# Performance work log

Measured on AMD Instinct MI355X. Metric: run time of the kernel, lower is better.

## Reference

```python
import math
import jax, jax.numpy as jnp
import numpy as np

# dims (from init_kwargs / forward signature)
B, N, K = 8, 1024, 8            # batch, nodes, num_neighbors
NC, TED, TEC = 64, 128, 64      # num_channels, time_embedding_dim, time_embedding_channels
C = NC + TEC                    # model dim = 128
H, Dh = 8, 16                   # heads, dim_head
HD = H * Dh
L = 4                           # num_layers
RH = 32                         # radial-net hidden width
NPATH = 10                      # radial scalars: k00,k10,k01,k11a,k11b,v00,v10,v01,v11a,v11b


def _g(k, shape, fan_in):
    return jax.random.normal(k, shape, dtype=jnp.float32) / np.sqrt(float(fan_in))


def setup_inputs() -> dict:
    key = jax.random.key(0)
    ks = jax.random.split(key, 16)
    return dict(
        x=jax.random.normal(ks[0], (B, N, 3), dtype=jnp.float32),
        y=jax.random.normal(ks[1], (B, N, 3), dtype=jnp.float32),
        t=jax.random.uniform(ks[2], (B,), dtype=jnp.float32) * 1000.0,
        Wt1=_g(ks[3], (TED, TED), TED), bt1=jnp.zeros((TED,), jnp.float32),
        Wt2=_g(ks[4], (TED, TEC), TED), bt2=jnp.zeros((TEC,), jnp.float32),
        Win0=_g(ks[5], (TEC + 3, C), TEC + 3), bin0=jnp.zeros((C,), jnp.float32),
        Win1=_g(ks[6], (1, C), 1),
        Wqkv=_g(ks[7], (L, 12, C, HD), C),           # q0,q1,k00,k10,k01,k11a,k11b,v00,v10,v01,v11a,v11b
        Wr1=_g(ks[8], (L, 1, RH), 1), br1=jnp.zeros((L, RH), jnp.float32),
        Wr2=_g(ks[9], (L, RH, H * NPATH), RH), br2=jnp.zeros((L, H * NPATH), jnp.float32),
        Wo=_g(ks[10], (L, 2, HD, C), HD), bo=jnp.zeros((L, 2, C), jnp.float32),
        Wout=_g(ks[11], (3, C), C), bout=jnp.zeros((3,), jnp.float32),
    )


def _forward(x, y, t, Wt1, bt1, Wt2, bt2, Win0, bin0, Win1, Wqkv,
             Wr1, br1, Wr2, br2, Wo, bo, Wout, bout):
    b, n = x.shape[0], x.shape[1]
    # sinusoidal time embedding + time MLP
    half = TED // 2
    freqs = jnp.exp(-math.log(10000.0) * jnp.arange(half, dtype=x.dtype) / half)
    emb = t[:, None] * freqs
    temb = jnp.concatenate([jnp.sin(emb), jnp.cos(emb)], axis=-1)          # [B,TED]
    temb = jax.nn.silu(temb @ Wt1 + bt1) @ Wt2 + bt2                        # [B,TEC]

    # degree-0 input = [time_embed | coords], degree-1 input = coords (1 channel)
    deg0 = jnp.concatenate([jnp.broadcast_to(temb[:, None, :], (b, n, TEC)), x], axis=-1)
    f0 = deg0 @ Win0 + bin0                                                 # [B,N,C]
    f1 = jnp.einsum('bnv,c->bncv', x, Win1[0])                              # [B,N,C,3]

    # k-nearest-neighbor graph on coordinates (shared across layers)
    d2 = jnp.sum((x[:, :, None, :] - x[:, None, :, :]) ** 2, axis=-1)       # [B,N,N]
    d2 = d2 + jnp.eye(n, dtype=x.dtype) * 1e9                               # exclude self
    _, idx = jax.lax.top_k(-d2, K)                                          # [B,N,K]
    gather = lambda f: jax.vmap(lambda a, i: a[i])(f, idx)                  # [B,N,...] -> [B,N,K,...]
    rel = gather(x) - x[:, :, None, :]                                      # [B,N,K,3]
    r = jnp.sqrt(jnp.sum(rel ** 2, axis=-1, keepdims=True) + 1e-8)          # [B,N,K,1]
    rhat = rel / r

    inv_scale = 1.0 / float(np.sqrt(2 * Dh))
    for l in range(L):
        Wl = Wqkv[l].reshape(12, C, H, Dh)
        q0 = jnp.einsum('bnc,chd->bnhd', f0, Wl[0])
        q1 = jnp.einsum('bncv,chd->bnhdv', f1, Wl[1])
        f0j, f1j = gather(f0), gather(f1)                                   # [B,N,K,C], [B,N,K,C,3]
        # radial network -> per-head, per-path scalars
        Rn = (jax.nn.silu(r @ Wr1[l] + br1[l]) @ Wr2[l] + br2[l]).reshape(b, n, K, H, NPATH)
        # equivariant tensor-product paths (degrees 0/1, spherical harmonics Y0,Y1,Y2)
        dot1 = jnp.einsum('bnkcv,bnkv->bnkc', f1j, rhat)                    # 1->0 path
        sym = 3.0 * dot1[..., None] * rhat[:, :, :, None, :] - f1j          # Y2 (traceless sym) 1->1 path
        p0 = lambda f, w: jnp.einsum('bnkc,chd->bnkhd', f, w)
        p1 = lambda f, w: jnp.einsum('bnkcv,chd->bnkhdv', f, w)
        rh = rhat[:, :, :, None, None, :]
        k0 = p0(f0j, Wl[2]) * Rn[..., 0:1] + p0(dot1, Wl[3]) * Rn[..., 1:2]
        k1 = (p0(f0j, Wl[4])[..., None] * rh * Rn[..., 2][..., None, None]
              + p1(f1j, Wl[5]) * Rn[..., 3][..., None, None]
              + p1(sym, Wl[6]) * Rn[..., 4][..., None, None])
        v0 = p0(f0j, Wl[7]) * Rn[..., 5:6] + p0(dot1, Wl[8]) * Rn[..., 6:7]
        v1 = (p0(f0j, Wl[9])[..., None] * rh * Rn[..., 7][..., None, None]
              + p1(f1j, Wl[10]) * Rn[..., 8][..., None, None]
              + p1(sym, Wl[11]) * Rn[..., 9][..., None, None])
        logits = (jnp.einsum('bnhd,bnkhd->bnhk', q0, k0)
                  + jnp.einsum('bnhdv,bnkhdv->bnhk', q1, k1)) * inv_scale
        attn = jax.nn.softmax(logits, axis=-1)
        o0 = jnp.einsum('bnhk,bnkhd->bnhd', attn, v0).reshape(b, n, HD)
        o1 = jnp.einsum('bnhk,bnkhdv->bnhdv', attn, v1).reshape(b, n, HD, 3)
        f0 = f0 + o0 @ Wo[l, 0] + bo[l, 0]
        f1 = f1 + jnp.einsum('bnev,ec->bncv', o1, Wo[l, 1]) + bo[l, 1][None, None, :, None]

    # output layer Linear(dim, 3) applied as per-component channel mixing on the type-1 output
    return jnp.einsum('bncv,vc->bnv', f1, Wout) + bout                      # [B,N,3]


def reference(x, y, t, Wt1, bt1, Wt2, bt2, Win0, bin0, Win1, Wqkv,
              Wr1, br1, Wr2, br2, Wo, bo, Wout, bout):
    return _forward(x, y, t, Wt1, bt1, Wt2, bt2, Win0, bin0, Win1, Wqkv,
                    Wr1, br1, Wr2, br2, Wo, bo, Wout, bout)
```

## Files before the change

kernel.cpp:

```cpp
#include <hip/hip_runtime.h>
#include <math.h>

#define NBATCH 8
#define NPTS   1024
#define KNN    8
#define CC     128
#define HD_    128
#define TED_   128
#define TEC_   64
#define RH     32
#define NL     4

typedef _Float16 half8 __attribute__((ext_vector_type(8)));
typedef _Float16 h4v  __attribute__((ext_vector_type(4)));
typedef float f32x4 __attribute__((ext_vector_type(4)));

__global__ __launch_bounds__(128) void k_temb(
    const float* __restrict__ t, const float* __restrict__ Wt1,
    const float* __restrict__ bt1, const float* __restrict__ Wt2,
    const float* __restrict__ bt2, const float* __restrict__ Win0,
    const float* __restrict__ bin0, float* __restrict__ pre0)
{
  int b = blockIdx.x;
  int tid = threadIdx.x;
  __shared__ float e128[TED_];
  __shared__ float h1[TED_];
  __shared__ float te[TEC_];
  float tv = t[b];
  if (tid < 64) {
    float fr = expf((-9.210340371976184f * (float)tid) * 0.015625f);
    float em = tv * fr;
    e128[tid]      = sinf(em);
    e128[tid + 64] = cosf(em);
  }
  __syncthreads();
  {
    float acc = bt1[tid];
    for (int i = 0; i < TED_; ++i) acc += e128[i] * Wt1[i * TED_ + tid];
    h1[tid] = acc / (1.0f + expf(-acc));
  }
  __syncthreads();
  if (tid < TEC_) {
    float acc = bt2[tid];
    for (int j = 0; j < TED_; ++j) acc += h1[j] * Wt2[j * TEC_ + tid];
    te[tid] = acc;
  }
  __syncthreads();
  {
    float acc = bin0[tid];
    for (int i = 0; i < TEC_; ++i) acc += te[i] * Win0[i * CC + tid];
    pre0[b * CC + tid] = acc;
  }
}

__global__ __launch_bounds__(256) void k_init(
    const float* __restrict__ x, const float* __restrict__ Win0,
    const float* __restrict__ Win1, const float* __restrict__ pre0,
    float* __restrict__ f0, float* __restrict__ f1,
    _Float16* __restrict__ f0h, _Float16* __restrict__ f1h)
{
  int node = blockIdx.x * 2 + (threadIdx.x >> 7);
  int c = threadIdx.x & 127;
  int b = node >> 10;
  float x0 = x[node * 3 + 0], x1 = x[node * 3 + 1], x2 = x[node * 3 + 2];
  float acc = pre0[b * CC + c]
            + x0 * Win0[(TEC_ + 0) * CC + c]
            + x1 * Win0[(TEC_ + 1) * CC + c]
            + x2 * Win0[(TEC_ + 2) * CC + c];
  f0[(size_t)node * CC + c] = acc;
  f0h[(size_t)node * CC + c] = (_Float16)acc;
  float w1 = Win1[c];
  float v0 = x0 * w1, v1 = x1 * w1, v2 = x2 * w1;
  f1[((size_t)node * 3 + 0) * CC + c] = v0;
  f1[((size_t)node * 3 + 1) * CC + c] = v1;
  f1[((size_t)node * 3 + 2) * CC + c] = v2;
  f1h[((size_t)node * 3 + 0) * CC + c] = (_Float16)v0;
  f1h[((size_t)node * 3 + 1) * CC + c] = (_Float16)v1;
  f1h[((size_t)node * 3 + 2) * CC + c] = (_Float16)v2;
}

__global__ __launch_bounds__(256) void k_knn(
    const float* __restrict__ x, int* __restrict__ idx,
    float* __restrict__ rhat, float* __restrict__ rl)
{
  const int b    = blockIdx.x >> 8;
  const int tile = blockIdx.x & 255;
  const int tid  = threadIdx.x;
  const int qg   = tid >> 6;
  const int sub  = tid & 63;

  __shared__ float xsx[NPTS], xsy[NPTS], xsz[NPTS];

  for (int i = tid; i < NPTS; i += 256) {
    const float* xp = x + ((size_t)b * NPTS + i) * 3;
    xsx[i] = xp[0]; xsy[i] = xp[1]; xsz[i] = xp[2];
  }
  __syncthreads();

  const int n = tile * 4 + qg;
  const float qx = xsx[n], qy = xsy[n], qz = xsz[n];

  unsigned long long bd[KNN];
  #pragma unroll
  for (int k = 0; k < KNN; ++k) bd[k] = ~0ull;

  const int j0 = sub * 16;
  #pragma unroll
  for (int it = 0; it < 16; ++it) {
    int j = j0 + ((it + sub) & 15);
    float dx = qx - xsx[j];
    float dy = qy - xsy[j];
    float dz = qz - xsz[j];
    float s = __fadd_rn(__fadd_rn(__fmul_rn(dx, dx), __fmul_rn(dy, dy)),
                        __fmul_rn(dz, dz));
    if (j == n) s = 1.0e9f;
    unsigned long long key =
        ((unsigned long long)__float_as_uint(s) << 32) | (unsigned int)j;
    if (key < bd[KNN - 1]) {
      bd[KNN - 1] = key;
      #pragma unroll
      for (int q = KNN - 1; q > 0; --q) {
        if (bd[q] < bd[q - 1]) {
          unsigned long long tmp = bd[q]; bd[q] = bd[q - 1]; bd[q - 1] = tmp;
        }
      }
    }
  }

  unsigned long long res[KNN];
  #pragma unroll
  for (int r = 0; r < KNN; ++r) {
    unsigned long long m = bd[0];
    #pragma unroll
    for (int mk = 1; mk < 64; mk <<= 1) {
      unsigned long long o = (unsigned long long)__shfl_xor((long long)m, mk, 64);
      m = (o < m) ? o : m;
    }
    if (bd[0] == m) {
      #pragma unroll
      for (int q = 0; q < KNN - 1; ++q) bd[q] = bd[q + 1];
      bd[KNN - 1] = ~0ull;
    }
    res[r] = m;
  }

  if (sub < KNN) {
    unsigned long long key = res[0];
    #pragma unroll
    for (int r = 1; r < KNN; ++r) if (sub == r) key = res[r];
    int j = (int)(key & 0xffffffffu);
    size_t base = ((size_t)b * NPTS + n) * KNN + sub;
    idx[base] = j;
    float rx = xsx[j] - qx;
    float ry = xsy[j] - qy;
    float rz = xsz[j] - qz;
    float rr2 = rx * rx + ry * ry + rz * rz + 1e-8f;
    float r = sqrtf(rr2);
    rl[base] = r;
    rhat[base * 3 + 0] = rx / r;
    rhat[base * 3 + 1] = ry / r;
    rhat[base * 3 + 2] = rz / r;
  }
}

__global__ __launch_bounds__(256) void k_rn(
    const float* __restrict__ rl, const float* __restrict__ Wr1,
    const float* __restrict__ br1, const float* __restrict__ Wr2,
    const float* __restrict__ br2, _Float16* __restrict__ Rn)
{
  const int l = blockIdx.y;
  const int e0 = blockIdx.x * 64;
  const int t = threadIdx.x;
  __shared__ _Float16 hid[64][48];
  __shared__ _Float16 wt[80][48];
  __shared__ _Float16 rn_lds[64][128];

  {
    uint4 zz = {0, 0, 0, 0};
    #pragma unroll
    for (int u = 0; u < 4; ++u)
      *(uint4*)((char*)rn_lds + (u * 256 + t) * 16) = zz;
  }
  {
    const float* wr2 = Wr2 + l * RH * 80;
    for (int i = t; i < 2560; i += 256) {
      int n = i >> 5, k = i & 31;
      wt[n][k] = (_Float16)wr2[k * 80 + n];
    }
  }
  {
    const float* wr1 = Wr1 + l * RH;
    const float* wb1 = br1 + l * RH;
    int e = t >> 2, i0 = (t & 3) * 8;
    float rv = rl[e0 + e];
    #pragma unroll
    for (int q = 0; q < 8; ++q) {
      int i = i0 + q;
      float zv = rv * wr1[i] + wb1[i];
      hid[e][i] = (_Float16)(zv / (1.0f + expf(-zv)));
    }
  }
  __syncthreads();

  {
    const int lane = t & 63;
    const int w = t >> 6;
    const int r15 = lane & 15;
    const int g = lane >> 4;
    half8 af = *(const half8*)&hid[w * 16 + r15][g * 8];
    const float* wb2 = br2 + l * 80;
    #pragma unroll
    for (int nt = 0; nt < 5; ++nt) {
      half8 bf = *(const half8*)&wt[nt * 16 + r15][g * 8];
      f32x4 acc = {};
      acc = __builtin_amdgcn_mfma_f32_16x16x32_f16(af, bf, acc, 0, 0, 0);
      int col = nt * 16 + r15;
      int hh = col / 10, j = col - hh * 10;
      float bv = wb2[col];
      #pragma unroll
      for (int i = 0; i < 4; ++i) {
        int e = w * 16 + g * 4 + i;
        rn_lds[e][hh * 16 + j] = (_Float16)(acc[i] + bv);
      }
    }
  }
  __syncthreads();
  _Float16* dst = Rn + ((size_t)l * 65536 + e0) * 128;
  #pragma unroll
  for (int u = 0; u < 4; ++u) {
    int i = u * 256 + t;
    *(uint4*)(dst + i * 8) = *(const uint4*)((const char*)rn_lds + i * 16);
  }
}

__global__ __launch_bounds__(256) void k_wconv(
    const float* __restrict__ Wqkv, const float* __restrict__ Wo,
    _Float16* __restrict__ Whq, _Float16* __restrict__ Who)
{
  __shared__ _Float16 T[128][136];
  int m = blockIdx.x;
  const float* src; _Float16* dst;
  if (m < 48) { src = Wqkv + (size_t)m * 16384; dst = Whq + (size_t)m * 16384; }
  else { src = Wo + (size_t)(m - 48) * 16384; dst = Who + (size_t)(m - 48) * 16384; }
  int tid = threadIdx.x;
  for (int i = tid; i < 16384; i += 256) {
    int k = i >> 7, n = i & 127;
    T[n][k] = (_Float16)src[i];
  }
  __syncthreads();
  for (int i = tid; i < 16384; i += 256) {
    int n = i >> 7, k = i & 127;
    dst[i] = T[n][k];
  }
}

#define MFMA_BODY(A_, ROWBASE_, WT_)                                          \
  const int tid  = threadIdx.x;                                               \
  const int lane = tid & 63;                                                  \
  const int w    = tid >> 6;                                                  \
  const int r15  = lane & 15;                                                 \
  const int g    = lane >> 4;                                                 \
  half8 bf[2][4];                                                             \
  _Pragma("unroll")                                                           \
  for (int ntl = 0; ntl < 2; ++ntl) {                                         \
    int n = (w * 2 + ntl) * 16 + r15;                                         \
    const _Float16* wp = (WT_) + (size_t)n * 128 + g * 8;                     \
    _Pragma("unroll")                                                         \
    for (int ks = 0; ks < 4; ++ks)                                            \
      bf[ntl][ks] = *(const half8*)(wp + ks * 32);                            \
  }                                                                           \
  {                                                                           \
    int r = tid >> 1;                                                         \
    const _Float16* src = (A_) + (size_t)((ROWBASE_) + r) * 128;              \
    int c0 = (tid & 1) * 8;                                                   \
    _Pragma("unroll")                                                         \
    for (int q = 0; q < 8; ++q) {                                             \
      int c = c0 + q;                                                         \
      *(uint4*)&As[r][c * 8] = *(const uint4*)(src + c * 8);                  \
    }                                                                         \
  }                                                                           \
  __syncthreads();                                                            \
  f32x4 acc[8][2] = {};                                                       \
  _Pragma("unroll")                                                           \
  for (int ks = 0; ks < 4; ++ks) {                                            \
    half8 a[8];                                                               \
    _Pragma("unroll")                                                         \
    for (int mt = 0; mt < 8; ++mt)                                            \
      a[mt] = *(const half8*)&As[mt * 16 + r15][ks * 32 + g * 8];             \
    _Pragma("unroll")                                                         \
    for (int mt = 0; mt < 8; ++mt) {                                          \
      acc[mt][0] = __builtin_amdgcn_mfma_f32_16x16x32_f16(bf[0][ks], a[mt], acc[mt][0], 0, 0, 0); \
      acc[mt][1] = __builtin_amdgcn_mfma_f32_16x16x32_f16(bf[1][ks], a[mt], acc[mt][1], 0, 0, 0); \
    }                                                                         \
  }

__global__ __launch_bounds__(256) void k_proj_mfma(
    const _Float16* __restrict__ f0h, const _Float16* __restrict__ f1h,
    const _Float16* __restrict__ Wh, _Float16* __restrict__ P0,
    _Float16* __restrict__ P1, int nb0)
{
  __shared__ _Float16 As[128][136];
  int z = blockIdx.x;
  const _Float16* A; const _Float16* Wt; _Float16* P; int ldP, colBase, rowBase;
  if (z < nb0 * 5) {
    const int map0[5] = {0, 2, 4, 7, 9};
    int m = z / nb0, rb = z - m * nb0;
    A = f0h; rowBase = rb * 128;
    Wt = Wh + (size_t)map0[m] * 16384;
    P = P0; ldP = 640; colBase = m * 128;
  } else {
    z -= nb0 * 5;
    int nb1 = nb0 * 3;
    const int map1[7] = {1, 3, 5, 6, 8, 10, 11};
    int m = z / nb1, rb = z - m * nb1;
    A = f1h; rowBase = rb * 128;
    Wt = Wh + (size_t)map1[m] * 16384;
    P = P1; ldP = 896; colBase = m * 128;
  }
  MFMA_BODY(A, rowBase, Wt)
  #pragma unroll
  for (int mt = 0; mt < 8; ++mt) {
    int row = rowBase + mt * 16 + r15;
    #pragma unroll
    for (int ntl = 0; ntl < 2; ++ntl) {
      int col = colBase + (w * 2 + ntl) * 16 + g * 4;
      h4v o;
      #pragma unroll
      for (int i = 0; i < 4; ++i) o[i] = (_Float16)acc[mt][ntl][i];
      *(h4v*)(P + (size_t)row * ldP + col) = o;
    }
  }
}

__global__ __launch_bounds__(256) void k_wo_mfma(
    const _Float16* __restrict__ o0h, const _Float16* __restrict__ o1h,
    const _Float16* __restrict__ Who_l, const float* __restrict__ bo_l,
    float* __restrict__ f0, float* __restrict__ f1,
    _Float16* __restrict__ f0h, _Float16* __restrict__ f1h, int nb0)
{
  __shared__ _Float16 As[128][136];
  int z = blockIdx.x;
  const _Float16* A; const _Float16* Wt; const float* bias;
  float* F; _Float16* FH; int rowBase;
  if (z < nb0) {
    A = o0h; Wt = Who_l; bias = bo_l; F = f0; FH = f0h; rowBase = z * 128;
  } else {
    z -= nb0;
    A = o1h; Wt = Who_l + 16384; bias = bo_l + CC; F = f1; FH = f1h; rowBase = z * 128;
  }
  MFMA_BODY(A, rowBase, Wt)
  #pragma unroll
  for (int mt = 0; mt < 8; ++mt) {
    int row = rowBase + mt * 16 + r15;
    #pragma unroll
    for (int ntl = 0; ntl < 2; ++ntl) {
      int col = (w * 2 + ntl) * 16 + g * 4;
      float4 bv = *(const float4*)&bias[col];
      float* fp = F + (size_t)row * 128 + col;
      _Float16* fhp = FH + (size_t)row * 128 + col;
      float4 fv = *(float4*)fp;
      fv.x += acc[mt][ntl][0] + bv.x;
      fv.y += acc[mt][ntl][1] + bv.y;
      fv.z += acc[mt][ntl][2] + bv.z;
      fv.w += acc[mt][ntl][3] + bv.w;
      *(float4*)fp = fv;
      h4v hh;
      hh[0] = (_Float16)fv.x; hh[1] = (_Float16)fv.y;
      hh[2] = (_Float16)fv.z; hh[3] = (_Float16)fv.w;
      *(h4v*)fhp = hh;
    }
  }
}

__global__ __launch_bounds__(256) void k_attn(
    const _Float16* __restrict__ P0, const _Float16* __restrict__ P1,
    const int* __restrict__ idx, const float* __restrict__ rhat,
    const _Float16* __restrict__ RnL,
    _Float16* __restrict__ o0h, _Float16* __restrict__ o1h,
    int nodeBase, int nbg)
{
  const int t = threadIdx.x;
  const int wv = t >> 6;
  const int lane = t & 63;
  const int cl = lane & 31;
  const int nh = lane >> 5;
  const int z = blockIdx.x;
  const int bb = z % nbg;
  const int qbase = (z / nbg) * 4;
  const int nodeLocal = bb * NPTS + qbase + wv;
  const int node = nodeBase + nodeLocal;
  const int batchRow = bb * NPTS;

  __shared__ float rh_s[4][KNN][3];
  if (t < 96) {
    int nd = t / 24, e = t % 24;
    rh_s[nd][e / 3][e % 3] =
        rhat[((size_t)(nodeBase + bb * NPTS + qbase + nd)) * KNN * 3 + e];
  }
  __syncthreads();

  const int c0 = cl * 4;
  const int h = cl >> 2;
  const _Float16* p0n = P0 + (size_t)nodeLocal * 640 + c0;
  const _Float16* p1n = P1 + (size_t)nodeLocal * 2688 + c0;
  h4v q0v  = *(const h4v*)(p0n);
  h4v q1xv = *(const h4v*)(p1n);
  h4v q1yv = *(const h4v*)(p1n + 896);
  h4v q1zv = *(const h4v*)(p1n + 1792);

  const float inv_scale = 0.17677669529663687f;
  const int* idxp = idx + (size_t)node * KNN + nh * 4;
  int jls[4];
  #pragma unroll
  for (int k = 0; k < 4; ++k) jls[k] = batchRow + idxp[k];
  const _Float16* rnp = RnL + ((size_t)node * KNN + nh * 4) * 128 + h * 16;

  float m = -3.0e38f, ssum = 0.0f;
  float a0[4] = {}, ax[4] = {}, ay[4] = {}, az[4] = {};

  for (int k = 0; k < 4; ++k) {
    int kk = nh * 4 + k;
    int jl = jls[k];
    const _Float16* g0 = P0 + (size_t)jl * 640 + c0;
    const _Float16* g1 = P1 + (size_t)jl * 2688 + c0;
    float rx = rh_s[wv][kk][0], ry = rh_s[wv][kk][1], rz = rh_s[wv][kk][2];

    half8 rv = *(const half8*)(rnp + (size_t)k * 128);
    h4v rv2 = *(const h4v*)(rnp + (size_t)k * 128 + 8);
    float r0 = (float)rv[0], r1 = (float)rv[1], r2 = (float)rv[2], r3 = (float)rv[3];
    float r4 = (float)rv[4], r5 = (float)rv[5], r6 = (float)rv[6], r7 = (float)rv[7];
    float r8 = (float)rv2[0], r9 = (float)rv2[1];

    float pl = 0.0f;
    {
      h4v G02 = *(const h4v*)(g0 + 128), G04 = *(const h4v*)(g0 + 256);
      h4v G13x = *(const h4v*)(g1 + 128),  G13y = *(const h4v*)(g1 + 896 + 128),  G13z = *(const h4v*)(g1 + 1792 + 128);
      h4v G15x = *(const h4v*)(g1 + 256),  G15y = *(const h4v*)(g1 + 896 + 256),  G15z = *(const h4v*)(g1 + 1792 + 256);
      h4v G16x = *(const h4v*)(g1 + 384),  G16y = *(const h4v*)(g1 + 896 + 384),  G16z = *(const h4v*)(g1 + 1792 + 384);
      #pragma unroll
      for (int ci = 0; ci < 4; ++ci) {
        float g02 = (float)G02[ci], g04 = (float)G04[ci];
        float g13x = (float)G13x[ci], g13y = (float)G13y[ci], g13z = (float)G13z[ci];
        float g15x = (float)G15x[ci], g15y = (float)G15y[ci], g15z = (float)G15z[ci];
        float g16x = (float)G16x[ci], g16y = (float)G16y[ci], g16z = (float)G16z[ci];
        float DP3 = g13x * rx + g13y * ry + g13z * rz;
        float DP6 = g16x * rx + g16y * ry + g16z * rz;
        float k0  = g02 * r0 + DP3 * r1;
        float k1x = g04 * rx * r2 + g15x * r3 + (3.0f * rx * DP6 - g16x) * r4;
        float k1y = g04 * ry * r2 + g15y * r3 + (3.0f * ry * DP6 - g16y) * r4;
        float k1z = g04 * rz * r2 + g15z * r3 + (3.0f * rz * DP6 - g16z) * r4;
        pl += (float)q0v[ci] * k0 + (float)q1xv[ci] * k1x
            + (float)q1yv[ci] * k1y + (float)q1zv[ci] * k1z;
      }
    }
    pl += __shfl_xor(pl, 1, 4);
    pl += __shfl_xor(pl, 2, 4);
    pl *= inv_scale;

    float mnew = fmaxf(m, pl);
    float scale = expf(m - mnew);
    float wgt = expf(pl - mnew);
    ssum = ssum * scale + wgt;
    m = mnew;

    {
      h4v G07 = *(const h4v*)(g0 + 384), G09 = *(const h4v*)(g0 + 512);
      h4v G18x = *(const h4v*)(g1 + 512),  G18y = *(const h4v*)(g1 + 896 + 512),  G18z = *(const h4v*)(g1 + 1792 + 512);
      h4v G1Ax = *(const h4v*)(g1 + 640),  G1Ay = *(const h4v*)(g1 + 896 + 640),  G1Az = *(const h4v*)(g1 + 1792 + 640);
      h4v G1Bx = *(const h4v*)(g1 + 768),  G1By = *(const h4v*)(g1 + 896 + 768),  G1Bz = *(const h4v*)(g1 + 1792 + 768);
      #pragma unroll
      for (int ci = 0; ci < 4; ++ci) {
        float g07 = (float)G07[ci], g09 = (float)G09[ci];
        float g18x = (float)G18x[ci], g18y = (float)G18y[ci], g18z = (float)G18z[ci];
        float g1ax = (float)G1Ax[ci], g1ay = (float)G1Ay[ci], g1az = (float)G1Az[ci];
        float g1bx = (float)G1Bx[ci], g1by = (float)G1By[ci], g1bz = (float)G1Bz[ci];
        float DP8 = g18x * rx + g18y * ry + g18z * rz;
        float DPB = g1bx * rx + g1by * ry + g1bz * rz;
        float v0  = g07 * r5 + DP8 * r6;
        float v1x = g09 * rx * r7 + g1ax * r8 + (3.0f * rx * DPB - g1bx) * r9;
        float v1y = g09 * ry * r7 + g1ay * r8 + (3.0f * ry * DPB - g1by) * r9;
        float v1z = g09 * rz * r7 + g1az * r8 + (3.0f * rz * DPB - g1bz) * r9;
        a0[ci] = a0[ci] * scale + wgt * v0;
        ax[ci] = ax[ci] * scale + wgt * v1x;
        ay[ci] = ay[ci] * scale + wgt * v1y;
        az[ci] = az[ci] * scale + wgt * v1z;
      }
    }
  }

  {
    float mo = __shfl_xor(m, 32, 64);
    float so = __shfl_xor(ssum, 32, 64);
    float mn = fmaxf(m, mo);
    float s_self = expf(m - mn);
    float s_oth  = expf(mo - mn);
    ssum = ssum * s_self + so * s_oth;
    #pragma unroll
    for (int ci = 0; ci < 4; ++ci) {
      float o0 = __shfl_xor(a0[ci], 32, 64);
      float ox = __shfl_xor(ax[ci], 32, 64);
      float oy = __shfl_xor(ay[ci], 32, 64);
      float oz = __shfl_xor(az[ci], 32, 64);
      a0[ci] = a0[ci] * s_self + o0 * s_oth;
      ax[ci] = ax[ci] * s_self + ox * s_oth;
      ay[ci] = ay[ci] * s_self + oy * s_oth;
      az[ci] = az[ci] * s_self + oz * s_oth;
    }
  }

  if (nh == 0) {
    float invs = 1.0f / ssum;
    h4v o;
    #pragma unroll
    for (int ci = 0; ci < 4; ++ci) o[ci] = (_Float16)(a0[ci] * invs);
    *(h4v*)(o0h + (size_t)nodeLocal * 128 + c0) = o;
    #pragma unroll
    for (int ci = 0; ci < 4; ++ci) o[ci] = (_Float16)(ax[ci] * invs);
    *(h4v*)(o1h + ((size_t)nodeLocal * 3 + 0) * 128 + c0) = o;
    #pragma unroll
    for (int ci = 0; ci < 4; ++ci) o[ci] = (_Float16)(ay[ci] * invs);
    *(h4v*)(o1h + ((size_t)nodeLocal * 3 + 1) * 128 + c0) = o;
    #pragma unroll
    for (int ci = 0; ci < 4; ++ci) o[ci] = (_Float16)(az[ci] * invs);
    *(h4v*)(o1h + ((size_t)nodeLocal * 3 + 2) * 128 + c0) = o;
  }
}

__global__ __launch_bounds__(256) void k_out(
    const float* __restrict__ f1, const float* __restrict__ Wout,
    const float* __restrict__ bout, float* __restrict__ out)
{
  int i = blockIdx.x * 256 + threadIdx.x;
  int v = i % 3;
  const float* row = f1 + (size_t)i * CC;
  const float* w = Wout + v * CC;
  float acc = 0.0f;
  #pragma unroll
  for (int c = 0; c < CC; c += 4) {
    float4 fv = *(const float4*)&row[c];
    float4 wv = *(const float4*)&w[c];
    acc += fv.x * wv.x + fv.y * wv.y + fv.z * wv.z + fv.w * wv.w;
  }
  out[i] = acc + bout[v];
}

extern "C" void kernel_launch(void* const* d_in, const int* in_sizes, int n_in,
                              void* d_out, int out_size, void* d_ws, size_t ws_size,
                              hipStream_t stream) {
  const float* x    = (const float*)d_in[0];
  const float* t    = (const float*)d_in[2];
  const float* Wt1  = (const float*)d_in[3];
  const float* bt1  = (const float*)d_in[4];
  const float* Wt2  = (const float*)d_in[5];
  const float* bt2  = (const float*)d_in[6];
  const float* Win0 = (const float*)d_in[7];
  const float* bin0 = (const float*)d_in[8];
  const float* Win1 = (const float*)d_in[9];
  const float* Wqkv = (const float*)d_in[10];
  const float* Wr1  = (const float*)d_in[11];
  const float* br1  = (const float*)d_in[12];
  const float* Wr2  = (const float*)d_in[13];
  const float* br2  = (const float*)d_in[14];
  const float* Wo   = (const float*)d_in[15];
  const float* bo   = (const float*)d_in[16];
  const float* Wout = (const float*)d_in[17];
  const float* bout = (const float*)d_in[18];
  float* out = (float*)d_out;

  char* wsb = (char*)d_ws;
  size_t off = 0;
  auto alloc = [&](size_t bytes) -> void* {
    void* p = wsb + off;
    off = (off + bytes + 255) & ~(size_t)255;
    return p;
  };
  const int totalNodes = NBATCH * NPTS;
  float* pre0 = (float*)alloc((size_t)NBATCH * CC * 4);
  float* f0   = (float*)alloc((size_t)totalNodes * CC * 4);
  float* f1   = (float*)alloc((size_t)totalNodes * 3 * CC * 4);
  _Float16* f0h = (_Float16*)alloc((size_t)totalNodes * CC * 2);
  _Float16* f1h = (_Float16*)alloc((size_t)totalNodes * 3 * CC * 2);
  _Float16* Whq = (_Float16*)alloc((size_t)NL * 12 * CC * HD_ * 2);
  _Float16* Who = (_Float16*)alloc((size_t)NL * 2 * CC * HD_ * 2);
  int*   idx  = (int*)alloc((size_t)totalNodes * KNN * 4);
  float* rhat = (float*)alloc((size_t)totalNodes * KNN * 3 * 4);
  float* rl   = (float*)alloc((size_t)totalNodes * KNN * 4);
  _Float16* Rn = (_Float16*)alloc((size_t)NL * totalNodes * KNN * 128 * 2);
  size_t fixedBytes = off;
  size_t perBatch = (size_t)NPTS * ((640 + 2688) * 2 + (128 + 384) * 2);
  int nbg = 8;
  while (nbg > 1 && fixedBytes + (size_t)nbg * perBatch + 8192 > ws_size) nbg >>= 1;
  _Float16* P0  = (_Float16*)alloc((size_t)nbg * NPTS * 640 * 2);
  _Float16* P1  = (_Float16*)alloc((size_t)nbg * NPTS * 2688 * 2);
  _Float16* o0h = (_Float16*)alloc((size_t)nbg * NPTS * 128 * 2);
  _Float16* o1h = (_Float16*)alloc((size_t)nbg * NPTS * 384 * 2);

  k_temb<<<NBATCH, 128, 0, stream>>>(t, Wt1, bt1, Wt2, bt2, Win0, bin0, pre0);
  k_init<<<totalNodes / 2, 256, 0, stream>>>(x, Win0, Win1, pre0, f0, f1, f0h, f1h);
  k_knn<<<NBATCH * 256, 256, 0, stream>>>(x, idx, rhat, rl);
  k_wconv<<<56, 256, 0, stream>>>(Wqkv, Wo, Whq, Who);
  k_rn<<<dim3(totalNodes * KNN / 64, NL), 256, 0, stream>>>(rl, Wr1, br1, Wr2, br2, Rn);

  for (int g = 0; g < NBATCH / nbg; ++g) {
    int nodeBase = g * nbg * NPTS;
    int nodes = nbg * NPTS;
    int nb0 = nodes / 128;
    for (int l = 0; l < NL; ++l) {
      k_proj_mfma<<<nb0 * 26, 256, 0, stream>>>(
          f0h + (size_t)nodeBase * CC, f1h + (size_t)nodeBase * 3 * CC,
          Whq + (size_t)l * 12 * CC * HD_, P0, P1, nb0);
      k_attn<<<nodes / 4, 256, 0, stream>>>(
          P0, P1, idx, rhat, Rn + (size_t)l * totalNodes * KNN * 128,
          o0h, o1h, nodeBase, nbg);
      k_wo_mfma<<<nb0 * 4, 256, 0, stream>>>(
          o0h, o1h, Who + (size_t)l * 2 * CC * HD_, bo + (size_t)(l * 2) * CC,
          f0 + (size_t)nodeBase * CC, f1 + (size_t)nodeBase * 3 * CC,
          f0h + (size_t)nodeBase * CC, f1h + (size_t)nodeBase * 3 * CC, nb0);
    }
  }
  k_out<<<(totalNodes * 3) / 256, 256, 0, stream>>>(f1, Wout, bout, out);
}
```

Measured before the change: 377.8 us.

## Split attention into logit/softmax and value-aggregation kernels

Splits the fused online-softmax attention kernel in two. The first kernel computes logits and normalized softmax weights into a small float buffer. The second kernel gathers values and accumulates them with those precomputed weights. The k-loops are fully unrolled, so more gathered loads can be in flight and the serial online-softmax rescaling goes away. In exchange it adds a kernel launch per layer, a round trip of the weight buffer through memory, and a second read of the index and rhat data.

```diff
diff --git a/kernel.cpp b/kernel.cpp
--- a/kernel.cpp
+++ b/kernel.cpp
@@ -372,11 +372,10 @@
   }
 }
 
-__global__ __launch_bounds__(256) void k_attn(
+__global__ __launch_bounds__(256) void k_attnA(
     const _Float16* __restrict__ P0, const _Float16* __restrict__ P1,
     const int* __restrict__ idx, const float* __restrict__ rhat,
-    const _Float16* __restrict__ RnL,
-    _Float16* __restrict__ o0h, _Float16* __restrict__ o1h,
+    const _Float16* __restrict__ RnL, float* __restrict__ Wgt,
     int nodeBase, int nbg)
 {
   const int t = threadIdx.x;
@@ -415,9 +414,8 @@
   for (int k = 0; k < 4; ++k) jls[k] = batchRow + idxp[k];
   const _Float16* rnp = RnL + ((size_t)node * KNN + nh * 4) * 128 + h * 16;
 
-  float m = -3.0e38f, ssum = 0.0f;
-  float a0[4] = {}, ax[4] = {}, ay[4] = {}, az[4] = {};
-
+  float pls[4];
+  #pragma unroll
   for (int k = 0; k < 4; ++k) {
     int kk = nh * 4 + k;
     int jl = jls[k];
@@ -426,102 +424,151 @@
     float rx = rh_s[wv][kk][0], ry = rh_s[wv][kk][1], rz = rh_s[wv][kk][2];
 
     half8 rv = *(const half8*)(rnp + (size_t)k * 128);
-    h4v rv2 = *(const h4v*)(rnp + (size_t)k * 128 + 8);
-    float r0 = (float)rv[0], r1 = (float)rv[1], r2 = (float)rv[2], r3 = (float)rv[3];
-    float r4 = (float)rv[4], r5 = (float)rv[5], r6 = (float)rv[6], r7 = (float)rv[7];
-    float r8 = (float)rv2[0], r9 = (float)rv2[1];
+    float r0 = (float)rv[0], r1 = (float)rv[1], r2 = (float)rv[2];
+    float r3 = (float)rv[3], r4 = (float)rv[4];
+
+    h4v G02 = *(const h4v*)(g0 + 128), G04 = *(const h4v*)(g0 + 256);
+    h4v G13x = *(const h4v*)(g1 + 128),  G13y = *(const h4v*)(g1 + 1024),  G13z = *(const h4v*)(g1 + 1920);
+    h4v G15x = *(const h4v*)(g1 + 256),  G15y = *(const h4v*)(g1 + 1152),  G15z = *(const h4v*)(g1 + 2048);
+    h4v G16x = *(const h4v*)(g1 + 384),  G16y = *(const h4v*)(g1 + 1280),  G16z = *(const h4v*)(g1 + 2176);
 
     float pl = 0.0f;
-    {
-      h4v G02 = *(const h4v*)(g0 + 128), G04 = *(const h4v*)(g0 + 256);
-      h4v G13x = *(const h4v*)(g1 + 128),  G13y = *(const h4v*)(g1 + 896 + 128),  G13z = *(const h4v*)(g1 + 1792 + 128);
-      h4v G15x = *(const h4v*)(g1 + 256),  G15y = *(const h4v*)(g1 + 896 + 256),  G15z = *(const h4v*)(g1 + 1792 + 256);
-      h4v G16x = *(const h4v*)(g1 + 384),  G16y = *(const h4v*)(g1 + 896 + 384),  G16z = *(const h4v*)(g1 + 1792 + 384);
-      #pragma unroll
-      for (int ci = 0; ci < 4; ++ci) {
-        float g02 = (float)G02[ci], g04 = (float)G04[ci];
-        float g13x = (float)G13x[ci], g13y = (float)G13y[ci], g13z = (float)G13z[ci];
-        float g15x = (float)G15x[ci], g15y = (float)G15y[ci], g15z = (float)G15z[ci];
-        float g16x = (float)G16x[ci], g16y = (float)G16y[ci], g16z = (float)G16z[ci];
-        float DP3 = g13x * rx + g13y * ry + g13z * rz;
-        float DP6 = g16x * rx + g16y * ry + g16z * rz;
-        float k0  = g02 * r0 + DP3 * r1;
-        float k1x = g04 * rx * r2 + g15x * r3 + (3.0f * rx * DP6 - g16x) * r4;
-        float k1y = g04 * ry * r2 + g15y * r3 + (3.0f * ry * DP6 - g16y) * r4;
-        float k1z = g04 * rz * r2 + g15z * r3 + (3.0f * rz * DP6 - g16z) * r4;
-        pl += (float)q0v[ci] * k0 + (float)q1xv[ci] * k1x
-            + (float)q1yv[ci] * k1y + (float)q1zv[ci] * k1z;
-      }
+    #pragma unroll
+    for (int ci = 0; ci < 4; ++ci) {
+      float g02 = (float)G02[ci], g04 = (float)G04[ci];
+      float g13x = (float)G13x[ci], g13y = (float)G13y[ci], g13z = (float)G13z[ci];
+      float g15x = (float)G15x[ci], g15y = (float)G15y[ci], g15z = (float)G15z[ci];
+      float g16x = (float)G16x[ci], g16y = (float)G16y[ci], g16z = (float)G16z[ci];
+      float DP3 = g13x * rx + g13y * ry + g13z * rz;
+      float DP6 = g16x * rx + g16y * ry + g16z * rz;
+      float k0  = g02 * r0 + DP3 * r1;
+      float k1x = g04 * rx * r2 + g15x * r3 + (3.0f * rx * DP6 - g16x) * r4;
+      float k1y = g04 * ry * r2 + g15y * r3 + (3.0f * ry * DP6 - g16y) * r4;
+      float k1z = g04 * rz * r2 + g15z * r3 + (3.0f * rz * DP6 - g16z) * r4;
+      pl += (float)q0v[ci] * k0 + (float)q1xv[ci] * k1x
+          + (float)q1yv[ci] * k1y + (float)q1zv[ci] * k1z;
     }
     pl += __shfl_xor(pl, 1, 4);
     pl += __shfl_xor(pl, 2, 4);
-    pl *= inv_scale;
-
-    float mnew = fmaxf(m, pl);
-    float scale = expf(m - mnew);
-    float wgt = expf(pl - mnew);
-    ssum = ssum * scale + wgt;
-    m = mnew;
-
-    {
-      h4v G07 = *(const h4v*)(g0 + 384), G09 = *(const h4v*)(g0 + 512);
-      h4v G18x = *(const h4v*)(g1 + 512),  G18y = *(const h4v*)(g1 + 896 + 512),  G18z = *(const h4v*)(g1 + 1792 + 512);
-      h4v G1Ax = *(const h4v*)(g1 + 640),  G1Ay = *(const h4v*)(g1 + 896 + 640),  G1Az = *(const h4v*)(g1 + 1792 + 640);
-      h4v G1Bx = *(const h4v*)(g1 + 768),  G1By = *(const h4v*)(g1 + 896 + 768),  G1Bz = *(const h4v*)(g1 + 1792 + 768);
-      #pragma unroll
-      for (int ci = 0; ci < 4; ++ci) {
-        float g07 = (float)G07[ci], g09 = (float)G09[ci];
-        float g18x = (float)G18x[ci], g18y = (float)G18y[ci], g18z = (float)G18z[ci];
-        float g1ax = (float)G1Ax[ci], g1ay = (float)G1Ay[ci], g1az = (float)G1Az[ci];
-        float g1bx = (float)G1Bx[ci], g1by = (float)G1By[ci], g1bz = (float)G1Bz[ci];
-        float DP8 = g18x * rx + g18y * ry + g18z * rz;
-        float DPB = g1bx * rx + g1by * ry + g1bz * rz;
-        float v0  = g07 * r5 + DP8 * r6;
-        float v1x = g09 * rx * r7 + g1ax * r8 + (3.0f * rx * DPB - g1bx) * r9;
-        float v1y = g09 * ry * r7 + g1ay * r8 + (3.0f * ry * DPB - g1by) * r9;
-        float v1z = g09 * rz * r7 + g1az * r8 + (3.0f * rz * DPB - g1bz) * r9;
-        a0[ci] = a0[ci] * scale + wgt * v0;
-        ax[ci] = ax[ci] * scale + wgt * v1x;
-        ay[ci] = ay[ci] * scale + wgt * v1y;
-        az[ci] = az[ci] * scale + wgt * v1z;
-      }
-    }
-  }
-
-  {
-    float mo = __shfl_xor(m, 32, 64);
-    float so = __shfl_xor(ssum, 32, 64);
-    float mn = fmaxf(m, mo);
-    float s_self = expf(m - mn);
-    float s_oth  = expf(mo - mn);
-    ssum = ssum * s_self + so * s_oth;
+    pls[k] = pl * inv_scale;
+  }
+
+  float mh = fmaxf(fmaxf(pls[0], pls[1]), fmaxf(pls[2], pls[3]));
+  float w0 = expf(pls[0] - mh), w1 = expf(pls[1] - mh);
+  float w2 = expf(pls[2] - mh), w3 = expf(pls[3] - mh);
+  float sh = w0 + w1 + w2 + w3;
+
+  float mo = __shfl_xor(mh, 32, 64);
+  float so = __shfl_xor(sh, 32, 64);
+  float mt_ = fmaxf(mh, mo);
+  float st = sh * expf(mh - mt_) + so * expf(mo - mt_);
+  float factor = expf(mh - mt_) / st;
+
+  if ((cl & 3) == 0) {
+    float4 wq;
+    wq.x = w0 * factor; wq.y = w1 * factor;
+    wq.z = w2 * factor; wq.w = w3 * factor;
+    *(float4*)(Wgt + (size_t)nodeLocal * 64 + h * 8 + nh * 4) = wq;
+  }
+}
+
+__global__ __launch_bounds__(256) void k_attnB(
+    const _Float16* __restrict__ P0, const _Float16* __restrict__ P1,
+    const int* __restrict__ idx, const float* __restrict__ rhat,
+    const _Float16* __restrict__ RnL, const float* __restrict__ Wgt,
+    _Float16* __restrict__ o0h, _Float16* __restrict__ o1h,
+    int nodeBase, int nbg)
+{
+  const int t = threadIdx.x;
+  const int wv = t >> 6;
+  const int lane = t & 63;
+  const int cl = lane & 31;
+  const int nh = lane >> 5;
+  const int z = blockIdx.x;
+  const int bb = z % nbg;
+  const int qbase = (z / nbg) * 4;
+  const int nodeLocal = bb * NPTS + qbase + wv;
+  const int node = nodeBase + nodeLocal;
+  const int batchRow = bb * NPTS;
+
+  __shared__ float rh_s[4][KNN][3];
+  if (t < 96) {
+    int nd = t / 24, e = t % 24;
+    rh_s[nd][e / 3][e % 3] =
+        rhat[((size_t)(nodeBase + bb * NPTS + qbase + nd)) * KNN * 3 + e];
+  }
+  __syncthreads();
+
+  const int c0 = cl * 4;
+  const int h = cl >> 2;
+  const int* idxp = idx + (size_t)node * KNN + nh * 4;
+  int jls[4];
+  #pragma unroll
+  for (int k = 0; k < 4; ++k) jls[k] = batchRow + idxp[k];
+  const _Float16* rnp = RnL + ((size_t)node * KNN + nh * 4) * 128 + h * 16;
+  float4 wq = *(const float4*)(Wgt + (size_t)nodeLocal * 64 + h * 8 + nh * 4);
+
+  float a0[4] = {}, ax[4] = {}, ay[4] = {}, az[4] = {};
+
+  #pragma unroll
+  for (int k = 0; k < 4; ++k) {
+    int kk = nh * 4 + k;
+    int jl = jls[k];
+    const _Float16* g0 = P0 + (size_t)jl * 640 + c0;
+    const _Float16* g1 = P1 + (size_t)jl * 2688 + c0;
+    float rx = rh_s[wv][kk][0], ry = rh_s[wv][kk][1], rz = rh_s[wv][kk][2];
+
+    half8 rv = *(const half8*)(rnp + (size_t)k * 128);
+    h4v rv2 = *(const h4v*)(rnp + (size_t)k * 128 + 8);
+    float r5 = (float)rv[5], r6 = (float)rv[6], r7 = (float)rv[7];
+    float r8 = (float)rv2[0], r9 = (float)rv2[1];
+    float wk = (k == 0) ? wq.x : (k == 1) ? wq.y : (k == 2) ? wq.z : wq.w;
+
+    h4v G07 = *(const h4v*)(g0 + 384), G09 = *(const h4v*)(g0 + 512);
+    h4v G18x = *(const h4v*)(g1 + 512),  G18y = *(const h4v*)(g1 + 1408),  G18z = *(const h4v*)(g1 + 2304);
+    h4v G1Ax = *(const h4v*)(g1 + 640),  G1Ay = *(const h4v*)(g1 + 1536),  G1Az = *(const h4v*)(g1 + 2432);
+    h4v G1Bx = *(const h4v*)(g1 + 768),  G1By = *(const h4v*)(g1 + 1664),  G1Bz = *(const h4v*)(g1 + 2560);
+
     #pragma unroll
     for (int ci = 0; ci < 4; ++ci) {
-      float o0 = __shfl_xor(a0[ci], 32, 64);
-      float ox = __shfl_xor(ax[ci], 32, 64);
-      float oy = __shfl_xor(ay[ci], 32, 64);
-      float oz = __shfl_xor(az[ci], 32, 64);
-      a0[ci] = a0[ci] * s_self + o0 * s_oth;
-      ax[ci] = ax[ci] * s_self + ox * s_oth;
-      ay[ci] = ay[ci] * s_self + oy * s_oth;
-      az[ci] = az[ci] * s_self + oz * s_oth;
-    }
+      float g07 = (float)G07[ci], g09 = (float)G09[ci];
+      float g18x = (float)G18x[ci], g18y = (float)G18y[ci], g18z = (float)G18z[ci];
+      float g1ax = (float)G1Ax[ci], g1ay = (float)G1Ay[ci], g1az = (float)G1Az[ci];
+      float g1bx = (float)G1Bx[ci], g1by = (float)G1By[ci], g1bz = (float)G1Bz[ci];
+      float DP8 = g18x * rx + g18y * ry + g18z * rz;
+      float DPB = g1bx * rx + g1by * ry + g1bz * rz;
+      float v0  = g07 * r5 + DP8 * r6;
+      float v1x = g09 * rx * r7 + g1ax * r8 + (3.0f * rx * DPB - g1bx) * r9;
+      float v1y = g09 * ry * r7 + g1ay * r8 + (3.0f * ry * DPB - g1by) * r9;
+      float v1z = g09 * rz * r7 + g1az * r8 + (3.0f * rz * DPB - g1bz) * r9;
+      a0[ci] += wk * v0;
+      ax[ci] += wk * v1x;
+      ay[ci] += wk * v1y;
+      az[ci] += wk * v1z;
+    }
+  }
+
+  #pragma unroll
+  for (int ci = 0; ci < 4; ++ci) {
+    a0[ci] += __shfl_xor(a0[ci], 32, 64);
+    ax[ci] += __shfl_xor(ax[ci], 32, 64);
+    ay[ci] += __shfl_xor(ay[ci], 32, 64);
+    az[ci] += __shfl_xor(az[ci], 32, 64);
   }
 
   if (nh == 0) {
-    float invs = 1.0f / ssum;
     h4v o;
     #pragma unroll
-    for (int ci = 0; ci < 4; ++ci) o[ci] = (_Float16)(a0[ci] * invs);
+    for (int ci = 0; ci < 4; ++ci) o[ci] = (_Float16)a0[ci];
     *(h4v*)(o0h + (size_t)nodeLocal * 128 + c0) = o;
     #pragma unroll
-    for (int ci = 0; ci < 4; ++ci) o[ci] = (_Float16)(ax[ci] * invs);
+    for (int ci = 0; ci < 4; ++ci) o[ci] = (_Float16)ax[ci];
     *(h4v*)(o1h + ((size_t)nodeLocal * 3 + 0) * 128 + c0) = o;
     #pragma unroll
-    for (int ci = 0; ci < 4; ++ci) o[ci] = (_Float16)(ay[ci] * invs);
+    for (int ci = 0; ci < 4; ++ci) o[ci] = (_Float16)ay[ci];
     *(h4v*)(o1h + ((size_t)nodeLocal * 3 + 1) * 128 + c0) = o;
     #pragma unroll
-    for (int ci = 0; ci < 4; ++ci) o[ci] = (_Float16)(az[ci] * invs);
+    for (int ci = 0; ci < 4; ++ci) o[ci] = (_Float16)az[ci];
     *(h4v*)(o1h + ((size_t)nodeLocal * 3 + 2) * 128 + c0) = o;
   }
 }
@@ -587,13 +634,14 @@
   float* rl   = (float*)alloc((size_t)totalNodes * KNN * 4);
   _Float16* Rn = (_Float16*)alloc((size_t)NL * totalNodes * KNN * 128 * 2);
   size_t fixedBytes = off;
-  size_t perBatch = (size_t)NPTS * ((640 + 2688) * 2 + (128 + 384) * 2);
+  size_t perBatch = (size_t)NPTS * ((640 + 2688) * 2 + (128 + 384) * 2 + 64 * 4);
   int nbg = 8;
   while (nbg > 1 && fixedBytes + (size_t)nbg * perBatch + 8192 > ws_size) nbg >>= 1;
   _Float16* P0  = (_Float16*)alloc((size_t)nbg * NPTS * 640 * 2);
   _Float16* P1  = (_Float16*)alloc((size_t)nbg * NPTS * 2688 * 2);
   _Float16* o0h = (_Float16*)alloc((size_t)nbg * NPTS * 128 * 2);
   _Float16* o1h = (_Float16*)alloc((size_t)nbg * NPTS * 384 * 2);
+  float* Wgt = (float*)alloc((size_t)nbg * NPTS * 64 * 4);
 
   k_temb<<<NBATCH, 128, 0, stream>>>(t, Wt1, bt1, Wt2, bt2, Win0, bin0, pre0);
   k_init<<<totalNodes / 2, 256, 0, stream>>>(x, Win0, Win1, pre0, f0, f1, f0h, f1h);
@@ -609,9 +657,12 @@
       k_proj_mfma<<<nb0 * 26, 256, 0, stream>>>(
           f0h + (size_t)nodeBase * CC, f1h + (size_t)nodeBase * 3 * CC,
           Whq + (size_t)l * 12 * CC * HD_, P0, P1, nb0);
-      k_attn<<<nodes / 4, 256, 0, stream>>>(
+      k_attnA<<<nodes / 4, 256, 0, stream>>>(
           P0, P1, idx, rhat, Rn + (size_t)l * totalNodes * KNN * 128,
-          o0h, o1h, nodeBase, nbg);
+          Wgt, nodeBase, nbg);
+      k_attnB<<<nodes / 4, 256, 0, stream>>>(
+          P0, P1, idx, rhat, Rn + (size_t)l * totalNodes * KNN * 128,
+          Wgt, o0h, o1h, nodeBase, nbg);
       k_wo_mfma<<<nb0 * 4, 256, 0, stream>>>(
           o0h, o1h, Who + (size_t)l * 2 * CC * HD_, bo + (size_t)(l * 2) * CC,
           f0 + (size_t)nodeBase * CC, f1 + (size_t)nodeBase * 3 * CC,
```

Result: slower. 414.1 us (+9.6%).
